# Performance work log

Hardware: AMD Instinct MI355X
Metric: run time of the kernel (lower is better)

## Reference

```python
import jax, jax.numpy as jnp
import numpy as np

B = 512          # batch
T_STEPS = 32     # clip_length (loop runs T-1 = 32 times)
BELIEF = 1024
STATE = 256
HIDDEN = 1024
EMB = 1024
POSE_TILES = 1
MIN_STD = 0.1


def setup_inputs() -> dict:
    key = jax.random.key(0)
    ks = jax.random.split(key, 24)
    s = 0.02
    rn = lambda k, sh: (jax.random.normal(k, sh, dtype=jnp.float32) * s)
    d = {
        "prev_state": jax.random.normal(ks[0], (B, STATE), dtype=jnp.float32),
        "prev_belief": jax.random.normal(ks[1], (B, BELIEF), dtype=jnp.float32),
        "poses": jax.random.normal(ks[2], (T_STEPS, B, 6), dtype=jnp.float32),
        "observations": jax.random.normal(ks[3], (T_STEPS, B, EMB), dtype=jnp.float32),
        "post_noise": jax.random.normal(ks[4], (T_STEPS, B, STATE), dtype=jnp.float32),
        "prior_noise": jax.random.normal(ks[5], (T_STEPS, B, STATE), dtype=jnp.float32),
        # fc_embed_state: 2*state -> belief
        "w_es": rn(ks[6], (2 * STATE, BELIEF)), "b_es": jnp.zeros((BELIEF,), jnp.float32),
        # GRUCell(belief, belief); torch gate order r, z, n
        "w_ih": rn(ks[7], (BELIEF, 3 * BELIEF)), "w_hh": rn(ks[8], (BELIEF, 3 * BELIEF)),
        "b_ih": jnp.zeros((3 * BELIEF,), jnp.float32), "b_hh": jnp.zeros((3 * BELIEF,), jnp.float32),
        # fc_embed_belief_posterior: belief+emb -> hidden
        "w_ebpo": rn(ks[9], (BELIEF + EMB, HIDDEN)), "b_ebpo": jnp.zeros((HIDDEN,), jnp.float32),
        # fc_state_posterior: hidden -> 2*state
        "w_spo": rn(ks[10], (HIDDEN, 2 * STATE)), "b_spo": jnp.zeros((2 * STATE,), jnp.float32),
        # fc_embed_belief_prior: belief + 6*pose_tiles -> hidden
        "w_ebpr": rn(ks[11], (BELIEF + 6 * POSE_TILES, HIDDEN)), "b_ebpr": jnp.zeros((HIDDEN,), jnp.float32),
        # fc_state_prior: hidden -> 2*state
        "w_spr": rn(ks[12], (HIDDEN, 2 * STATE)), "b_spr": jnp.zeros((2 * STATE,), jnp.float32),
    }
    return d


def _rssm(prev_state, prev_belief, poses, observations, post_noise, prior_noise,
          w_es, b_es, w_ih, w_hh, b_ih, b_hh,
          w_ebpo, b_ebpo, w_spo, b_spo, w_ebpr, b_ebpr, w_spr, b_spr):
    def gru_cell(x, h):
        gi = x @ w_ih + b_ih
        gh = h @ w_hh + b_hh
        ir, iz, inn = jnp.split(gi, 3, axis=1)
        hr, hz, hn = jnp.split(gh, 3, axis=1)
        r = jax.nn.sigmoid(ir + hr)
        z = jax.nn.sigmoid(iz + hz)
        n = jnp.tanh(inn + r * hn)
        return (1.0 - z) * n + z * h

    def step(carry, xs):
        post_s, prior_s, belief = carry
        obs_t, pose_t, n_post, n_prior = xs
        hidden = jax.nn.relu(jnp.concatenate([post_s, prior_s], axis=1) @ w_es + b_es)
        belief = gru_cell(hidden, belief)
        # posterior branch
        hp = jax.nn.relu(jnp.concatenate([belief, obs_t], axis=1) @ w_ebpo + b_ebpo)
        pm, psd_raw = jnp.split(hp @ w_spo + b_spo, 2, axis=1)
        psd = jax.nn.softplus(psd_raw) + MIN_STD
        ps = pm + psd * n_post
        # prior branch (pose tiled)
        pose_rep = jnp.tile(pose_t, (1, POSE_TILES))
        hq = jax.nn.relu(jnp.concatenate([belief, pose_rep], axis=1) @ w_ebpr + b_ebpr)
        prm, prsd_raw = jnp.split(hq @ w_spr + b_spr, 2, axis=1)
        prsd = jax.nn.softplus(prsd_raw) + MIN_STD
        prs = prm + prsd * n_prior
        return (ps, prs, belief), (belief, prs, prm, prsd, ps, pm, psd)

    init = (prev_state, prev_state, prev_belief)
    _, outs = jax.lax.scan(step, init, (observations, poses, post_noise, prior_noise))
    # outs: beliefs, prior_states, prior_means, prior_std_devs, posterior_states, posterior_means, posterior_std_devs  (each [T-1, B, *])
    return outs


def reference(prev_state, prev_belief, poses, observations, post_noise, prior_noise,
              w_es, b_es, w_ih, w_hh, b_ih, b_hh,
              w_ebpo, b_ebpo, w_spo, b_spo, w_ebpr, b_ebpr, w_spr, b_spr):
    return _rssm(prev_state, prev_belief, poses, observations, post_noise, prior_noise,
                 w_es, b_es, w_ih, w_hh, b_ih, b_hh,
                 w_ebpo, b_ebpo, w_spo, b_spo, w_ebpr, b_ebpr, w_spr, b_spr)
```

## Files before the change

### kernel.cpp

```cpp
#include <hip/hip_runtime.h>
#include <math.h>


typedef __attribute__((ext_vector_type(8))) short bf16x8;
typedef __attribute__((ext_vector_type(4))) float f32x4;

#define MFMA(a, b, c) __builtin_amdgcn_mfma_f32_16x16x32_bf16(a, b, c, 0, 0, 0)
#define NBLK 256

__device__ __forceinline__ short f2bf(float f) {
    unsigned u = __float_as_uint(f);
    u += 0x7FFF + ((u >> 16) & 1);
    return (short)(u >> 16);
}
__device__ __forceinline__ float sigmoidf_(float x) { return 1.f / (1.f + expf(-x)); }
__device__ __forceinline__ float softplusf_(float x) {
    return fmaxf(x, 0.f) + log1pf(expf(-fabsf(x)));
}
__device__ __forceinline__ f32x4 zero4() { f32x4 v = {0.f, 0.f, 0.f, 0.f}; return v; }

__global__ __launch_bounds__(256) void k_swizzle(const float* __restrict__ W,
                                                 short* __restrict__ out,
                                                 int KT, int N)
{
    int gw = blockIdx.x * 4 + (threadIdx.x >> 6);
    int lane = threadIdx.x & 63;
    int nt = gw / KT, kt = gw % KT;
    const float* src = W + (size_t)(kt * 32 + (lane >> 4) * 8) * N + nt * 16 + (lane & 15);
    short tmp[8];
#pragma unroll
    for (int j = 0; j < 8; ++j) tmp[j] = f2bf(src[(size_t)j * N]);
    *(bf16x8*)(out + (((size_t)gw * 64 + lane) << 3)) = *(const bf16x8*)tmp;
}

__global__ __launch_bounds__(256) void k_obs2bf(const float* __restrict__ obs,
                                                short* __restrict__ out)
{
    size_t i = ((size_t)blockIdx.x * 256 + threadIdx.x) * 8;
    short tmp[8];
#pragma unroll
    for (int j = 0; j < 8; ++j) tmp[j] = f2bf(obs[i + j]);
    *(bf16x8*)(out + i) = *(const bf16x8*)tmp;
}

__global__ __launch_bounds__(256) void k_init(const float* __restrict__ prev_state,
                                              const float* __restrict__ prev_belief,
                                              short* __restrict__ stateCat0,
                                              short* __restrict__ belInit,
                                              unsigned* __restrict__ bar)
{
    int i = blockIdx.x * 256 + threadIdx.x;
    if (i < 4096) bar[i] = 0u;
    if (i < 262144) {
        int m = i >> 9, c = i & 511;
        stateCat0[i] = f2bf(prev_state[m * 256 + (c & 255)]);
    } else {
        int j = i - 262144;
        belInit[j] = f2bf(prev_belief[j]);
    }
}

__device__ __forceinline__ bf16x8 loadA16(const short* A, int m0, int kelem, int strideElems, int lane) {
    return *(const bf16x8*)(A + (size_t)(m0 + (lane & 15)) * strideElems + kelem + ((lane >> 4) << 3));
}
__device__ __forceinline__ bf16x8 loadB16(const short* Bsw, size_t tileIdx, int lane) {
    return *(const bf16x8*)(Bsw + ((tileIdx * 64 + lane) << 3));
}

__device__ __forceinline__ void xbar(unsigned* cnt, unsigned target)
{
    __syncthreads();
    if (threadIdx.x == 0) {
        __hip_atomic_fetch_add(cnt, 1u, __ATOMIC_RELAXED, __HIP_MEMORY_SCOPE_AGENT);
        while (__hip_atomic_load(cnt, __ATOMIC_RELAXED, __HIP_MEMORY_SCOPE_AGENT) < target)
            __builtin_amdgcn_s_sleep(4);
    }
    __syncthreads();
}

struct RP2 {
    const short *sw_es, *sw_ih, *sw_hh, *sw_ebpo, *sw_ebpr, *sw_spo, *sw_spr;
    const float *Wf_ebpr;
    const float *b_es, *b_ih, *b_hh, *b_ebpo, *b_ebpr, *b_spo, *b_spr;
    const float *prev_belief, *poses, *post_noise, *prior_noise;
    const short *obsBf;
    const short *belInit;
    short *hiddenB, *belB, *hpB, *hqB, *scB;
    float *beliefs, *priStates, *priMeans, *priStds, *postStates, *postMeans, *postStds;
    unsigned *bar;
};

__global__ __launch_bounds__(256, 1) void k_rssm2(RP2 p)
{
    int wid = threadIdx.x >> 6;
    int lane = threadIdx.x & 63;
    int q = lane >> 4, cl = lane & 15;

    __shared__ unsigned s_g, s_rank, s_P;
    if (threadIdx.x == 0) {
        unsigned x;
        asm volatile("s_getreg_b32 %0, hwreg(HW_REG_XCC_ID)" : "=s"(x));
        x &= 7u;
        s_g = x;
        s_rank = __hip_atomic_fetch_add(p.bar + 64 + x * 64, 1u,
                                        __ATOMIC_RELAXED, __HIP_MEMORY_SCOPE_AGENT);
    }
    __syncthreads();
    if (threadIdx.x == 0) {
        __hip_atomic_fetch_add(p.bar, 1u, __ATOMIC_RELAXED, __HIP_MEMORY_SCOPE_AGENT);
        while (__hip_atomic_load(p.bar, __ATOMIC_RELAXED, __HIP_MEMORY_SCOPE_AGENT) < NBLK)
            __builtin_amdgcn_s_sleep(4);
        s_P = __hip_atomic_load(p.bar + 64 + s_g * 64,
                                __ATOMIC_RELAXED, __HIP_MEMORY_SCOPE_AGENT);
    }
    __syncthreads();
    const unsigned g = s_g, P = s_P, rank = s_rank;
    const unsigned NSLOT = P * 4;
    const unsigned slot = rank * 4 + (unsigned)wid;
    const int R0 = (int)g * 64;
    unsigned* cnt = p.bar + 1024 + g * 64;
    unsigned bcount = 0;

#pragma unroll 1
    for (int t = 0; t < 32; ++t) {
        {
            const short* sc = p.scB + (size_t)t * 262144;
            short* hid = p.hiddenB + (size_t)t * 524288;
            for (unsigned u = slot; u < 128; u += NSLOT) {
                int mt = u >> 6, nt = u & 63;
                int m0 = R0 + mt * 32;
                f32x4 acc0 = zero4(), acc1 = zero4();
#pragma unroll 4
                for (int kt = 0; kt < 16; ++kt) {
                    bf16x8 a0 = loadA16(sc, m0,      kt * 32, 512, lane);
                    bf16x8 a1 = loadA16(sc, m0 + 16, kt * 32, 512, lane);
                    bf16x8 b  = loadB16(p.sw_es, (size_t)nt * 16 + kt, lane);
                    acc0 = MFMA(a0, b, acc0);
                    acc1 = MFMA(a1, b, acc1);
                }
                int n = nt * 16 + cl;
                float bn = p.b_es[n];
#pragma unroll
                for (int i = 0; i < 4; ++i) {
                    int m = m0 + q * 4 + i;
                    hid[(size_t)m * 1024 + n]        = f2bf(fmaxf(acc0[i] + bn, 0.f));
                    hid[(size_t)(m + 16) * 1024 + n] = f2bf(fmaxf(acc1[i] + bn, 0.f));
                }
            }
        }
        xbar(cnt, ++bcount * P);

        {
            const short* hid = p.hiddenB + (size_t)t * 524288;
            const short* belPrevBf = t ? p.belB + (size_t)(t - 1) * 524288 : p.belInit;
            const float* Pf32 = t ? (p.beliefs + (size_t)(t - 1) * 524288) : p.prev_belief;
            float* belT = p.beliefs + (size_t)t * 524288;
            short* belCurBf = p.belB + (size_t)t * 524288;
            for (unsigned u = slot; u < 128; u += NSLOT) {
                int mt = u >> 6, nt = u & 63;
                int m0 = R0 + mt * 32;
                f32x4 r0 = zero4(), r1 = zero4(), z0 = zero4(), z1 = zero4();
                f32x4 ni0 = zero4(), ni1 = zero4(), nh0 = zero4(), nh1 = zero4();
#pragma unroll 4
                for (int kt = 0; kt < 32; ++kt) {
                    bf16x8 a0 = loadA16(hid, m0,      kt * 32, 1024, lane);
                    bf16x8 a1 = loadA16(hid, m0 + 16, kt * 32, 1024, lane);
                    bf16x8 br = loadB16(p.sw_ih, (size_t)(0 * 64 + nt) * 32 + kt, lane);
                    bf16x8 bz = loadB16(p.sw_ih, (size_t)(1 * 64 + nt) * 32 + kt, lane);
                    bf16x8 bn = loadB16(p.sw_ih, (size_t)(2 * 64 + nt) * 32 + kt, lane);
                    r0 = MFMA(a0, br, r0);   r1 = MFMA(a1, br, r1);
                    z0 = MFMA(a0, bz, z0);   z1 = MFMA(a1, bz, z1);
                    ni0 = MFMA(a0, bn, ni0); ni1 = MFMA(a1, bn, ni1);
                }
#pragma unroll 4
                for (int kt = 0; kt < 32; ++kt) {
                    bf16x8 a0 = loadA16(belPrevBf, m0,      kt * 32, 1024, lane);
                    bf16x8 a1 = loadA16(belPrevBf, m0 + 16, kt * 32, 1024, lane);
                    bf16x8 br = loadB16(p.sw_hh, (size_t)(0 * 64 + nt) * 32 + kt, lane);
                    bf16x8 bz = loadB16(p.sw_hh, (size_t)(1 * 64 + nt) * 32 + kt, lane);
                    bf16x8 bn = loadB16(p.sw_hh, (size_t)(2 * 64 + nt) * 32 + kt, lane);
                    r0 = MFMA(a0, br, r0);   r1 = MFMA(a1, br, r1);
                    z0 = MFMA(a0, bz, z0);   z1 = MFMA(a1, bz, z1);
                    nh0 = MFMA(a0, bn, nh0); nh1 = MFMA(a1, bn, nh1);
                }
                int n = nt * 16 + cl;
                float bihr = p.b_ih[n] + p.b_hh[n];
                float bihz = p.b_ih[1024 + n] + p.b_hh[1024 + n];
                float bin = p.b_ih[2048 + n], bhn = p.b_hh[2048 + n];
#pragma unroll
                for (int f = 0; f < 2; ++f) {
#pragma unroll
                    for (int i = 0; i < 4; ++i) {
                        int m = m0 + f * 16 + q * 4 + i;
                        float rv = f ? r1[i] : r0[i];
                        float zv = f ? z1[i] : z0[i];
                        float niv = f ? ni1[i] : ni0[i];
                        float nhv = f ? nh1[i] : nh0[i];
                        float rr = sigmoidf_(rv + bihr);
                        float zz = sigmoidf_(zv + bihz);
                        float ng = tanhf(niv + bin + rr * (nhv + bhn));
                        float h = Pf32[(size_t)m * 1024 + n];
                        float v = (1.f - zz) * ng + zz * h;
                        belT[(size_t)m * 1024 + n] = v;
                        belCurBf[(size_t)m * 1024 + n] = f2bf(v);
                    }
                }
            }
        }
        xbar(cnt, ++bcount * P);

        {
            const short* belCur = p.belB + (size_t)t * 524288;
            const short* obsT = p.obsBf + (size_t)t * 524288;
            const float* poseT = p.poses + (size_t)t * 3072;
            short* hp = p.hpB + (size_t)t * 524288;
            short* hq = p.hqB + (size_t)t * 524288;
            for (unsigned u = slot; u < 256; u += NSLOT) {
                int u2 = u & 127;
                int mt = u2 >> 6, nt = u2 & 63;
                int m0 = R0 + mt * 32;
                if (u < 128) {
                    f32x4 acc0 = zero4(), acc1 = zero4();
#pragma unroll 4
                    for (int kt = 0; kt < 32; ++kt) {
                        bf16x8 a0 = loadA16(belCur, m0,      kt * 32, 1024, lane);
                        bf16x8 a1 = loadA16(belCur, m0 + 16, kt * 32, 1024, lane);
                        bf16x8 bb = loadB16(p.sw_ebpo, (size_t)nt * 64 + kt, lane);
                        acc0 = MFMA(a0, bb, acc0);
                        acc1 = MFMA(a1, bb, acc1);
                    }
#pragma unroll 4
                    for (int kt = 32; kt < 64; ++kt) {
                        bf16x8 a0 = loadA16(obsT, m0,      (kt - 32) * 32, 1024, lane);
                        bf16x8 a1 = loadA16(obsT, m0 + 16, (kt - 32) * 32, 1024, lane);
                        bf16x8 bb = loadB16(p.sw_ebpo, (size_t)nt * 64 + kt, lane);
                        acc0 = MFMA(a0, bb, acc0);
                        acc1 = MFMA(a1, bb, acc1);
                    }
                    int n = nt * 16 + cl;
                    float bn = p.b_ebpo[n];
#pragma unroll
                    for (int i = 0; i < 4; ++i) {
                        int m = m0 + q * 4 + i;
                        hp[(size_t)m * 1024 + n]        = f2bf(fmaxf(acc0[i] + bn, 0.f));
                        hp[(size_t)(m + 16) * 1024 + n] = f2bf(fmaxf(acc1[i] + bn, 0.f));
                    }
                } else {
                    f32x4 acc0 = zero4(), acc1 = zero4();
#pragma unroll 4
                    for (int kt = 0; kt < 32; ++kt) {
                        bf16x8 a0 = loadA16(belCur, m0,      kt * 32, 1024, lane);
                        bf16x8 a1 = loadA16(belCur, m0 + 16, kt * 32, 1024, lane);
                        bf16x8 bb = loadB16(p.sw_ebpr, (size_t)nt * 32 + kt, lane);
                        acc0 = MFMA(a0, bb, acc0);
                        acc1 = MFMA(a1, bb, acc1);
                    }
                    int n = nt * 16 + cl;
                    float bn2 = p.b_ebpr[n];
#pragma unroll
                    for (int f = 0; f < 2; ++f) {
#pragma unroll
                        for (int i = 0; i < 4; ++i) {
                            int m = m0 + f * 16 + q * 4 + i;
                            float v = (f ? acc1[i] : acc0[i]) + bn2;
#pragma unroll
                            for (int pp = 0; pp < 6; ++pp)
                                v += poseT[(size_t)m * 6 + pp] * p.Wf_ebpr[(size_t)(1024 + pp) * 1024 + n];
                            hq[(size_t)m * 1024 + n] = f2bf(fmaxf(v, 0.f));
                        }
                    }
                }
            }
        }
        xbar(cnt, ++bcount * P);

        {
            const short* hp = p.hpB + (size_t)t * 524288;
            const short* hq = p.hqB + (size_t)t * 524288;
            short* scW = p.scB + (size_t)(t + 1) * 262144;
            for (unsigned u = slot; u < 128; u += NSLOT) {
                int br = u >> 6;
                int rem = u & 63;
                int mtd = rem >> 4;
                int ct = rem & 15;
                int mh = R0 + mtd * 16;
                const short* A = br ? hq : hp;
                const short* Bsw = br ? p.sw_spr : p.sw_spo;
                const float* bias = br ? p.b_spr : p.b_spo;
                const float* noise = (br ? p.prior_noise : p.post_noise) + (size_t)t * 131072;
                float* mO  = (br ? p.priMeans  : p.postMeans)  + (size_t)t * 131072;
                float* sO  = (br ? p.priStds   : p.postStds)   + (size_t)t * 131072;
                float* stO = (br ? p.priStates : p.postStates) + (size_t)t * 131072;
                int catOff = br ? 256 : 0;
                f32x4 ma = zero4(), sa = zero4();
#pragma unroll 4
                for (int kt = 0; kt < 32; ++kt) {
                    bf16x8 a  = loadA16(A, mh, kt * 32, 1024, lane);
                    bf16x8 bm = loadB16(Bsw, (size_t)ct * 32 + kt, lane);
                    bf16x8 bs = loadB16(Bsw, (size_t)(16 + ct) * 32 + kt, lane);
                    ma = MFMA(a, bm, ma);
                    sa = MFMA(a, bs, sa);
                }
#pragma unroll
                for (int i = 0; i < 4; ++i) {
                    int m = mh + q * 4 + i;
                    int c = ct * 16 + cl;
                    float mean = ma[i] + bias[c];
                    float sd = softplusf_(sa[i] + bias[c + 256]) + 0.1f;
                    float st = mean + sd * noise[(size_t)m * 256 + c];
                    mO[(size_t)m * 256 + c] = mean;
                    sO[(size_t)m * 256 + c] = sd;
                    stO[(size_t)m * 256 + c] = st;
                    scW[(size_t)m * 512 + catOff + c] = f2bf(st);
                }
            }
        }
        xbar(cnt, ++bcount * P);
    }
}

__global__ __launch_bounds__(256) void k_embed_state(
    const short* __restrict__ A, const short* __restrict__ Bsw,
    const float* __restrict__ bias, short* __restrict__ outBf)
{
    int wid = threadIdx.x >> 6;
    int lane = threadIdx.x & 63;
    int nt = blockIdx.x & 63, mb = blockIdx.x >> 6;
    int m0 = (mb * 4 + wid) * 32;
    f32x4 acc0 = zero4(), acc1 = zero4();
#pragma unroll 4
    for (int kt = 0; kt < 16; ++kt) {
        bf16x8 a0 = loadA16(A, m0,      kt * 32, 512, lane);
        bf16x8 a1 = loadA16(A, m0 + 16, kt * 32, 512, lane);
        bf16x8 b  = loadB16(Bsw, (size_t)nt * 16 + kt, lane);
        acc0 = MFMA(a0, b, acc0);
        acc1 = MFMA(a1, b, acc1);
    }
    int q = lane >> 4, cl = lane & 15;
    int n = nt * 16 + cl;
    float bn = bias[n];
#pragma unroll
    for (int i = 0; i < 4; ++i) {
        int m = m0 + q * 4 + i;
        outBf[(size_t)m * 1024 + n]        = f2bf(fmaxf(acc0[i] + bn, 0.f));
        outBf[(size_t)(m + 16) * 1024 + n] = f2bf(fmaxf(acc1[i] + bn, 0.f));
    }
}

__global__ __launch_bounds__(256) void k_gru(
    const short* __restrict__ Hbf, const short* __restrict__ Pbf,
    const float* __restrict__ Pf32,
    const short* __restrict__ sw_ih, const short* __restrict__ sw_hh,
    const float* __restrict__ b_ih, const float* __restrict__ b_hh,
    float* __restrict__ belF32, short* __restrict__ belBf)
{
    int wid = threadIdx.x >> 6;
    int lane = threadIdx.x & 63;
    int nt = blockIdx.x & 63, mb = blockIdx.x >> 6;
    int m0 = (mb * 4 + wid) * 32;
    f32x4 r0 = zero4(), r1 = zero4(), z0 = zero4(), z1 = zero4();
    f32x4 ni0 = zero4(), ni1 = zero4(), nh0 = zero4(), nh1 = zero4();
#pragma unroll 4
    for (int kt = 0; kt < 32; ++kt) {
        bf16x8 a0 = loadA16(Hbf, m0,      kt * 32, 1024, lane);
        bf16x8 a1 = loadA16(Hbf, m0 + 16, kt * 32, 1024, lane);
        bf16x8 br = loadB16(sw_ih, (size_t)(0 * 64 + nt) * 32 + kt, lane);
        bf16x8 bz = loadB16(sw_ih, (size_t)(1 * 64 + nt) * 32 + kt, lane);
        bf16x8 bn = loadB16(sw_ih, (size_t)(2 * 64 + nt) * 32 + kt, lane);
        r0 = MFMA(a0, br, r0);   r1 = MFMA(a1, br, r1);
        z0 = MFMA(a0, bz, z0);   z1 = MFMA(a1, bz, z1);
        ni0 = MFMA(a0, bn, ni0); ni1 = MFMA(a1, bn, ni1);
    }
#pragma unroll 4
    for (int kt = 0; kt < 32; ++kt) {
        bf16x8 a0 = loadA16(Pbf, m0,      kt * 32, 1024, lane);
        bf16x8 a1 = loadA16(Pbf, m0 + 16, kt * 32, 1024, lane);
        bf16x8 br = loadB16(sw_hh, (size_t)(0 * 64 + nt) * 32 + kt, lane);
        bf16x8 bz = loadB16(sw_hh, (size_t)(1 * 64 + nt) * 32 + kt, lane);
        bf16x8 bn = loadB16(sw_hh, (size_t)(2 * 64 + nt) * 32 + kt, lane);
        r0 = MFMA(a0, br, r0);   r1 = MFMA(a1, br, r1);
        z0 = MFMA(a0, bz, z0);   z1 = MFMA(a1, bz, z1);
        nh0 = MFMA(a0, bn, nh0); nh1 = MFMA(a1, bn, nh1);
    }
    int q = lane >> 4, cl = lane & 15;
    int n = nt * 16 + cl;
    float bihr = b_ih[n] + b_hh[n];
    float bihz = b_ih[1024 + n] + b_hh[1024 + n];
    float bin = b_ih[2048 + n], bhn = b_hh[2048 + n];
#pragma unroll
    for (int f = 0; f < 2; ++f) {
#pragma unroll
        for (int i = 0; i < 4; ++i) {
            int m = m0 + f * 16 + q * 4 + i;
            float rv = f ? r1[i] : r0[i];
            float zv = f ? z1[i] : z0[i];
            float niv = f ? ni1[i] : ni0[i];
            float nhv = f ? nh1[i] : nh0[i];
            float rr = sigmoidf_(rv + bihr);
            float zz = sigmoidf_(zv + bihz);
            float ng = tanhf(niv + bin + rr * (nhv + bhn));
            float h = Pf32[(size_t)m * 1024 + n];
            float v = (1.f - zz) * ng + zz * h;
            belF32[(size_t)m * 1024 + n] = v;
            belBf[(size_t)m * 1024 + n] = f2bf(v);
        }
    }
}

__global__ __launch_bounds__(256) void k_pp(
    const short* __restrict__ Bel, const short* __restrict__ ObsBf,
    const float* __restrict__ Pose,
    const short* __restrict__ sw_ebpo, const short* __restrict__ sw_ebpr,
    const float* __restrict__ Wf_ebpr,
    const float* __restrict__ b_ebpo, const float* __restrict__ b_ebpr,
    short* __restrict__ hpBf, short* __restrict__ hqBf)
{
    int wid = threadIdx.x >> 6;
    int lane = threadIdx.x & 63;
    int q = lane >> 4, cl = lane & 15;
    int b = blockIdx.x;
    if (b < 256) {
        int nt = b & 63, mb = b >> 6;
        int m0 = (mb * 4 + wid) * 32;
        f32x4 acc0 = zero4(), acc1 = zero4();
#pragma unroll 4
        for (int kt = 0; kt < 32; ++kt) {
            bf16x8 a0 = loadA16(Bel, m0,      kt * 32, 1024, lane);
            bf16x8 a1 = loadA16(Bel, m0 + 16, kt * 32, 1024, lane);
            bf16x8 bb = loadB16(sw_ebpo, (size_t)nt * 64 + kt, lane);
            acc0 = MFMA(a0, bb, acc0);
            acc1 = MFMA(a1, bb, acc1);
        }
#pragma unroll 4
        for (int kt = 32; kt < 64; ++kt) {
            bf16x8 a0 = loadA16(ObsBf, m0,      (kt - 32) * 32, 1024, lane);
            bf16x8 a1 = loadA16(ObsBf, m0 + 16, (kt - 32) * 32, 1024, lane);
            bf16x8 bb = loadB16(sw_ebpo, (size_t)nt * 64 + kt, lane);
            acc0 = MFMA(a0, bb, acc0);
            acc1 = MFMA(a1, bb, acc1);
        }
        int n = nt * 16 + cl;
        float bn = b_ebpo[n];
#pragma unroll
        for (int i = 0; i < 4; ++i) {
            int m = m0 + q * 4 + i;
            hpBf[(size_t)m * 1024 + n]        = f2bf(fmaxf(acc0[i] + bn, 0.f));
            hpBf[(size_t)(m + 16) * 1024 + n] = f2bf(fmaxf(acc1[i] + bn, 0.f));
        }
    } else {
        int b2 = b - 256;
        int nt = b2 & 63, mb = b2 >> 6;
        int m0 = (mb * 4 + wid) * 32;
        f32x4 acc0 = zero4(), acc1 = zero4();
#pragma unroll 4
        for (int kt = 0; kt < 32; ++kt) {
            bf16x8 a0 = loadA16(Bel, m0,      kt * 32, 1024, lane);
            bf16x8 a1 = loadA16(Bel, m0 + 16, kt * 32, 1024, lane);
            bf16x8 bb = loadB16(sw_ebpr, (size_t)nt * 32 + kt, lane);
            acc0 = MFMA(a0, bb, acc0);
            acc1 = MFMA(a1, bb, acc1);
        }
        int n = nt * 16 + cl;
        float bn = b_ebpr[n];
#pragma unroll
        for (int f = 0; f < 2; ++f) {
#pragma unroll
            for (int i = 0; i < 4; ++i) {
                int m = m0 + f * 16 + q * 4 + i;
                float v = (f ? acc1[i] : acc0[i]) + bn;
#pragma unroll
                for (int pp = 0; pp < 6; ++pp)
                    v += Pose[(size_t)m * 6 + pp] * Wf_ebpr[(size_t)(1024 + pp) * 1024 + n];
                hqBf[(size_t)m * 1024 + n] = f2bf(fmaxf(v, 0.f));
            }
        }
    }
}

__global__ __launch_bounds__(256) void k_head(
    const short* __restrict__ Hp, const short* __restrict__ Hq,
    const short* __restrict__ sw_spo, const short* __restrict__ sw_spr,
    const float* __restrict__ b_spo, const float* __restrict__ b_spr,
    const float* __restrict__ nPost, const float* __restrict__ nPri,
    float* __restrict__ pM, float* __restrict__ pS, float* __restrict__ pSt,
    float* __restrict__ qM, float* __restrict__ qS, float* __restrict__ qSt,
    short* __restrict__ stateCat)
{
    int gw = blockIdx.x * 4 + (threadIdx.x >> 6);
    int lane = threadIdx.x & 63;
    int br = gw >> 9, rem = gw & 511;
    int mt = rem >> 4, ct = rem & 15;
    int m0 = mt * 16;
    const short* A = br ? Hq : Hp;
    const short* Bsw = br ? sw_spr : sw_spo;
    const float* bias = br ? b_spr : b_spo;
    const float* noise = br ? nPri : nPost;
    float* mO = br ? qM : pM;
    float* sO = br ? qS : pS;
    float* stO = br ? qSt : pSt;
    int catOff = br ? 256 : 0;
    f32x4 ma = zero4(), sa = zero4();
#pragma unroll 4
    for (int kt = 0; kt < 32; ++kt) {
        bf16x8 a = loadA16(A, m0, kt * 32, 1024, lane);
        bf16x8 bm = loadB16(Bsw, (size_t)ct * 32 + kt, lane);
        bf16x8 bs = loadB16(Bsw, (size_t)(16 + ct) * 32 + kt, lane);
        ma = MFMA(a, bm, ma);
        sa = MFMA(a, bs, sa);
    }
    int q = lane >> 4, cl = lane & 15;
#pragma unroll
    for (int i = 0; i < 4; ++i) {
        int m = m0 + q * 4 + i;
        int c = ct * 16 + cl;
        float mean = ma[i] + bias[c];
        float sd = softplusf_(sa[i] + bias[c + 256]) + 0.1f;
        float st = mean + sd * noise[(size_t)m * 256 + c];
        mO[(size_t)m * 256 + c] = mean;
        sO[(size_t)m * 256 + c] = sd;
        stO[(size_t)m * 256 + c] = st;
        stateCat[(size_t)m * 512 + catOff + c] = f2bf(st);
    }
}

extern "C" void kernel_launch(void* const* d_in, const int* in_sizes, int n_in,
                              void* d_out, int out_size, void* d_ws, size_t ws_size,
                              hipStream_t stream)
{
    const float* prev_state  = (const float*)d_in[0];
    const float* prev_belief = (const float*)d_in[1];
    const float* poses       = (const float*)d_in[2];
    const float* obs         = (const float*)d_in[3];
    const float* post_noise  = (const float*)d_in[4];
    const float* prior_noise = (const float*)d_in[5];
    const float* w_es   = (const float*)d_in[6];
    const float* b_es   = (const float*)d_in[7];
    const float* w_ih   = (const float*)d_in[8];
    const float* w_hh   = (const float*)d_in[9];
    const float* b_ih   = (const float*)d_in[10];
    const float* b_hh   = (const float*)d_in[11];
    const float* w_ebpo = (const float*)d_in[12];
    const float* b_ebpo = (const float*)d_in[13];
    const float* w_spo  = (const float*)d_in[14];
    const float* b_spo  = (const float*)d_in[15];
    const float* w_ebpr = (const float*)d_in[16];
    const float* b_ebpr = (const float*)d_in[17];
    const float* w_spr  = (const float*)d_in[18];
    const float* b_spr  = (const float*)d_in[19];

    float* out = (float*)d_out;
    float* beliefs    = out;
    float* priStates  = out + 16777216;
    float* priMeans   = out + 20971520;
    float* priStds    = out + 25165824;
    float* postStates = out + 29360128;
    float* postMeans  = out + 33554432;
    float* postStds   = out + 37748736;

    short* ws = (short*)d_ws;
    size_t o = 0;
    short* sw_es   = ws + o; o += (size_t)512 * 1024;
    short* sw_ih   = ws + o; o += (size_t)1024 * 3072;
    short* sw_hh   = ws + o; o += (size_t)1024 * 3072;
    short* sw_ebpo = ws + o; o += (size_t)2048 * 1024;
    short* sw_ebpr = ws + o; o += (size_t)1024 * 1024;
    short* sw_spo  = ws + o; o += (size_t)1024 * 512;
    short* sw_spr  = ws + o; o += (size_t)1024 * 512;
    short* obsBf   = ws + o; o += (size_t)32 * 512 * 1024;
    short* hiddenB = ws + o; o += (size_t)32 * 512 * 1024;
    short* belInit = ws + o; o += (size_t)512 * 1024;
    short* belB    = ws + o; o += (size_t)32 * 512 * 1024;
    short* hpB     = ws + o; o += (size_t)32 * 512 * 1024;
    short* hqB     = ws + o; o += (size_t)32 * 512 * 1024;
    short* scB     = ws + o; o += (size_t)33 * 512 * 512;
    unsigned* bar  = (unsigned*)(ws + o); o += 8192;

    k_swizzle<<<dim3(256),  dim3(256), 0, stream>>>(w_es,   sw_es,   16, 1024);
    k_swizzle<<<dim3(1536), dim3(256), 0, stream>>>(w_ih,   sw_ih,   32, 3072);
    k_swizzle<<<dim3(1536), dim3(256), 0, stream>>>(w_hh,   sw_hh,   32, 3072);
    k_swizzle<<<dim3(1024), dim3(256), 0, stream>>>(w_ebpo, sw_ebpo, 64, 1024);
    k_swizzle<<<dim3(512),  dim3(256), 0, stream>>>(w_ebpr, sw_ebpr, 32, 1024);
    k_swizzle<<<dim3(256),  dim3(256), 0, stream>>>(w_spo,  sw_spo,  32, 512);
    k_swizzle<<<dim3(256),  dim3(256), 0, stream>>>(w_spr,  sw_spr,  32, 512);
    k_obs2bf<<<dim3(8192), dim3(256), 0, stream>>>(obs, obsBf);
    k_init<<<dim3(3072), dim3(256), 0, stream>>>(prev_state, prev_belief, scB, belInit, bar);

    RP2 rp;
    rp.sw_es = sw_es; rp.sw_ih = sw_ih; rp.sw_hh = sw_hh;
    rp.sw_ebpo = sw_ebpo; rp.sw_ebpr = sw_ebpr; rp.sw_spo = sw_spo; rp.sw_spr = sw_spr;
    rp.Wf_ebpr = w_ebpr;
    rp.b_es = b_es; rp.b_ih = b_ih; rp.b_hh = b_hh;
    rp.b_ebpo = b_ebpo; rp.b_ebpr = b_ebpr; rp.b_spo = b_spo; rp.b_spr = b_spr;
    rp.prev_belief = prev_belief; rp.poses = poses;
    rp.post_noise = post_noise; rp.prior_noise = prior_noise;
    rp.obsBf = obsBf; rp.belInit = belInit;
    rp.hiddenB = hiddenB; rp.belB = belB; rp.hpB = hpB; rp.hqB = hqB; rp.scB = scB;
    rp.beliefs = beliefs;
    rp.priStates = priStates; rp.priMeans = priMeans; rp.priStds = priStds;
    rp.postStates = postStates; rp.postMeans = postMeans; rp.postStds = postStds;
    rp.bar = bar;

    void* kargs[] = { (void*)&rp };
    hipError_t ce = hipLaunchCooperativeKernel(k_rssm2, dim3(NBLK), dim3(256),
                                               kargs, 0u, stream);
    if (ce != hipSuccess) {
        for (int t = 0; t < 32; ++t) {
            const short* belPrevBf = t ? belB + (size_t)(t - 1) * 524288 : belInit;
            short* belCurBf = belB + (size_t)t * 524288;
            const float* belPrevF = t ? (beliefs + (size_t)(t - 1) * 524288) : prev_belief;
            float* belT = beliefs + (size_t)t * 524288;
            short* hid = hiddenB + (size_t)t * 524288;
            short* hp = hpB + (size_t)t * 524288;
            short* hq = hqB + (size_t)t * 524288;

            k_embed_state<<<dim3(256), dim3(256), 0, stream>>>(scB + (size_t)t * 262144,
                                                               sw_es, b_es, hid);
            k_gru<<<dim3(256), dim3(256), 0, stream>>>(hid, belPrevBf, belPrevF,
                                                       sw_ih, sw_hh, b_ih, b_hh, belT, belCurBf);
            k_pp<<<dim3(512), dim3(256), 0, stream>>>(belCurBf, obsBf + (size_t)t * 524288,
                                                      poses + (size_t)t * 3072,
                                                      sw_ebpo, sw_ebpr, w_ebpr,
                                                      b_ebpo, b_ebpr, hp, hq);
            k_head<<<dim3(256), dim3(256), 0, stream>>>(hp, hq, sw_spo, sw_spr, b_spo, b_spr,
                                                        post_noise + (size_t)t * 131072,
                                                        prior_noise + (size_t)t * 131072,
                                                        postMeans + (size_t)t * 131072,
                                                        postStds + (size_t)t * 131072,
                                                        postStates + (size_t)t * 131072,
                                                        priMeans + (size_t)t * 131072,
                                                        priStds + (size_t)t * 131072,
                                                        priStates + (size_t)t * 131072,
                                                        scB + (size_t)(t + 1) * 262144);
        }
    }
}
```

Baseline: 3.024 ms.

## Partition by output columns per XCD with hierarchical grid barrier and 512-thread blocks

The work split changes from per-XCD row partitions, each using all weight columns, to per-XCD column partitions covering all rows. Each XCD then streams only its own slice of the weights, which keeps those weights resident in its L2 cache. Because every step now needs data produced by other XCDs, the per-XCD barrier becomes a two-level grid barrier (local arrive, leader cross-XCD sync, local release), and intermediate stores use agent-scope atomic stores so other XCDs can see them. Block size doubles to 512 threads with 16-row MFMA tiles. In exchange, the A operand is no longer reused across two 16-row tiles, and each barrier now costs a global round trip.

```diff
diff --git a/kernel.cpp b/kernel.cpp
--- a/kernel.cpp
+++ b/kernel.cpp
@@ -18,6 +18,13 @@
     return fmaxf(x, 0.f) + log1pf(expf(-fabsf(x)));
 }
 __device__ __forceinline__ f32x4 zero4() { f32x4 v = {0.f, 0.f, 0.f, 0.f}; return v; }
+
+__device__ __forceinline__ void stS(short* p, short v) {
+    __hip_atomic_store(p, v, __ATOMIC_RELAXED, __HIP_MEMORY_SCOPE_AGENT);
+}
+__device__ __forceinline__ unsigned ldU(const unsigned* p) {
+    return __hip_atomic_load(p, __ATOMIC_RELAXED, __HIP_MEMORY_SCOPE_AGENT);
+}
 
 __global__ __launch_bounds__(256) void k_swizzle(const float* __restrict__ W,
                                                  short* __restrict__ out,
@@ -65,17 +72,6 @@
 }
 __device__ __forceinline__ bf16x8 loadB16(const short* Bsw, size_t tileIdx, int lane) {
     return *(const bf16x8*)(Bsw + ((tileIdx * 64 + lane) << 3));
-}
-
-__device__ __forceinline__ void xbar(unsigned* cnt, unsigned target)
-{
-    __syncthreads();
-    if (threadIdx.x == 0) {
-        __hip_atomic_fetch_add(cnt, 1u, __ATOMIC_RELAXED, __HIP_MEMORY_SCOPE_AGENT);
-        while (__hip_atomic_load(cnt, __ATOMIC_RELAXED, __HIP_MEMORY_SCOPE_AGENT) < target)
-            __builtin_amdgcn_s_sleep(4);
-    }
-    __syncthreads();
 }
 
 struct RP2 {
@@ -90,7 +86,28 @@
     unsigned *bar;
 };
 
-__global__ __launch_bounds__(256, 1) void k_rssm2(RP2 p)
+__device__ __forceinline__ void hbar(unsigned* bar, unsigned g, unsigned P,
+                                     unsigned rank, unsigned* bc)
+{
+    unsigned c = ++(*bc);
+    __syncthreads();
+    if (threadIdx.x == 0) {
+        unsigned* larr = bar + 1024 + g * 64;
+        unsigned* lrel = bar + 2048 + g * 64;
+        __hip_atomic_fetch_add(larr, 1u, __ATOMIC_RELAXED, __HIP_MEMORY_SCOPE_AGENT);
+        if (rank == 0) {
+            while (ldU(larr) < c * P) {}
+            __hip_atomic_fetch_add(bar + 8, 1u, __ATOMIC_RELAXED, __HIP_MEMORY_SCOPE_AGENT);
+            while (ldU(bar + 8) < c * 8u) {}
+            __hip_atomic_store(lrel, c, __ATOMIC_RELAXED, __HIP_MEMORY_SCOPE_AGENT);
+        } else {
+            while (ldU(lrel) < c) {}
+        }
+    }
+    __syncthreads();
+}
+
+__global__ __launch_bounds__(512, 1) void k_rssm3(RP2 p)
 {
     int wid = threadIdx.x >> 6;
     int lane = threadIdx.x & 63;
@@ -108,47 +125,40 @@
     __syncthreads();
     if (threadIdx.x == 0) {
         __hip_atomic_fetch_add(p.bar, 1u, __ATOMIC_RELAXED, __HIP_MEMORY_SCOPE_AGENT);
-        while (__hip_atomic_load(p.bar, __ATOMIC_RELAXED, __HIP_MEMORY_SCOPE_AGENT) < NBLK)
-            __builtin_amdgcn_s_sleep(4);
-        s_P = __hip_atomic_load(p.bar + 64 + s_g * 64,
-                                __ATOMIC_RELAXED, __HIP_MEMORY_SCOPE_AGENT);
+        while (ldU(p.bar) < NBLK) {}
+        s_P = ldU(p.bar + 64 + s_g * 64);
     }
     __syncthreads();
     const unsigned g = s_g, P = s_P, rank = s_rank;
-    const unsigned NSLOT = P * 4;
-    const unsigned slot = rank * 4 + (unsigned)wid;
-    const int R0 = (int)g * 64;
-    unsigned* cnt = p.bar + 1024 + g * 64;
-    unsigned bcount = 0;
+    const unsigned NSLOT = P * 8;
+    const unsigned slot = rank * 8 + (unsigned)wid;
+    unsigned bc = 0;
 
 #pragma unroll 1
     for (int t = 0; t < 32; ++t) {
         {
             const short* sc = p.scB + (size_t)t * 262144;
             short* hid = p.hiddenB + (size_t)t * 524288;
-            for (unsigned u = slot; u < 128; u += NSLOT) {
-                int mt = u >> 6, nt = u & 63;
-                int m0 = R0 + mt * 32;
-                f32x4 acc0 = zero4(), acc1 = zero4();
+            for (unsigned u = slot; u < 256; u += NSLOT) {
+                int mt = (int)(u >> 3), ntl = (int)(u & 7);
+                int nt = (int)g * 8 + ntl;
+                int m0 = mt * 16;
+                f32x4 acc = zero4();
 #pragma unroll 4
                 for (int kt = 0; kt < 16; ++kt) {
-                    bf16x8 a0 = loadA16(sc, m0,      kt * 32, 512, lane);
-                    bf16x8 a1 = loadA16(sc, m0 + 16, kt * 32, 512, lane);
-                    bf16x8 b  = loadB16(p.sw_es, (size_t)nt * 16 + kt, lane);
-                    acc0 = MFMA(a0, b, acc0);
-                    acc1 = MFMA(a1, b, acc1);
+                    bf16x8 a = loadA16(sc, m0, kt * 32, 512, lane);
+                    bf16x8 b = loadB16(p.sw_es, (size_t)nt * 16 + kt, lane);
+                    acc = MFMA(a, b, acc);
                 }
                 int n = nt * 16 + cl;
                 float bn = p.b_es[n];
 #pragma unroll
-                for (int i = 0; i < 4; ++i) {
-                    int m = m0 + q * 4 + i;
-                    hid[(size_t)m * 1024 + n]        = f2bf(fmaxf(acc0[i] + bn, 0.f));
-                    hid[(size_t)(m + 16) * 1024 + n] = f2bf(fmaxf(acc1[i] + bn, 0.f));
-                }
+                for (int i = 0; i < 4; ++i)
+                    stS(&hid[(size_t)(m0 + q * 4 + i) * 1024 + n],
+                        f2bf(fmaxf(acc[i] + bn, 0.f)));
             }
         }
-        xbar(cnt, ++bcount * P);
+        hbar(p.bar, g, P, rank, &bc);
 
         {
             const short* hid = p.hiddenB + (size_t)t * 524288;
@@ -156,58 +166,49 @@
             const float* Pf32 = t ? (p.beliefs + (size_t)(t - 1) * 524288) : p.prev_belief;
             float* belT = p.beliefs + (size_t)t * 524288;
             short* belCurBf = p.belB + (size_t)t * 524288;
-            for (unsigned u = slot; u < 128; u += NSLOT) {
-                int mt = u >> 6, nt = u & 63;
-                int m0 = R0 + mt * 32;
-                f32x4 r0 = zero4(), r1 = zero4(), z0 = zero4(), z1 = zero4();
-                f32x4 ni0 = zero4(), ni1 = zero4(), nh0 = zero4(), nh1 = zero4();
+            for (unsigned u = slot; u < 256; u += NSLOT) {
+                int mt = (int)(u >> 3), ntl = (int)(u & 7);
+                int nt = (int)g * 8 + ntl;
+                int m0 = mt * 16;
+                f32x4 r = zero4(), z = zero4(), ni = zero4(), nh = zero4();
 #pragma unroll 4
                 for (int kt = 0; kt < 32; ++kt) {
-                    bf16x8 a0 = loadA16(hid, m0,      kt * 32, 1024, lane);
-                    bf16x8 a1 = loadA16(hid, m0 + 16, kt * 32, 1024, lane);
+                    bf16x8 a  = loadA16(hid, m0, kt * 32, 1024, lane);
                     bf16x8 br = loadB16(p.sw_ih, (size_t)(0 * 64 + nt) * 32 + kt, lane);
                     bf16x8 bz = loadB16(p.sw_ih, (size_t)(1 * 64 + nt) * 32 + kt, lane);
                     bf16x8 bn = loadB16(p.sw_ih, (size_t)(2 * 64 + nt) * 32 + kt, lane);
-                    r0 = MFMA(a0, br, r0);   r1 = MFMA(a1, br, r1);
-                    z0 = MFMA(a0, bz, z0);   z1 = MFMA(a1, bz, z1);
-                    ni0 = MFMA(a0, bn, ni0); ni1 = MFMA(a1, bn, ni1);
+                    r = MFMA(a, br, r);
+                    z = MFMA(a, bz, z);
+                    ni = MFMA(a, bn, ni);
                 }
 #pragma unroll 4
                 for (int kt = 0; kt < 32; ++kt) {
-                    bf16x8 a0 = loadA16(belPrevBf, m0,      kt * 32, 1024, lane);
-                    bf16x8 a1 = loadA16(belPrevBf, m0 + 16, kt * 32, 1024, lane);
+                    bf16x8 a  = loadA16(belPrevBf, m0, kt * 32, 1024, lane);
                     bf16x8 br = loadB16(p.sw_hh, (size_t)(0 * 64 + nt) * 32 + kt, lane);
                     bf16x8 bz = loadB16(p.sw_hh, (size_t)(1 * 64 + nt) * 32 + kt, lane);
                     bf16x8 bn = loadB16(p.sw_hh, (size_t)(2 * 64 + nt) * 32 + kt, lane);
-                    r0 = MFMA(a0, br, r0);   r1 = MFMA(a1, br, r1);
-                    z0 = MFMA(a0, bz, z0);   z1 = MFMA(a1, bz, z1);
-                    nh0 = MFMA(a0, bn, nh0); nh1 = MFMA(a1, bn, nh1);
+                    r = MFMA(a, br, r);
+                    z = MFMA(a, bz, z);
+                    nh = MFMA(a, bn, nh);
                 }
                 int n = nt * 16 + cl;
                 float bihr = p.b_ih[n] + p.b_hh[n];
                 float bihz = p.b_ih[1024 + n] + p.b_hh[1024 + n];
                 float bin = p.b_ih[2048 + n], bhn = p.b_hh[2048 + n];
 #pragma unroll
-                for (int f = 0; f < 2; ++f) {
-#pragma unroll
-                    for (int i = 0; i < 4; ++i) {
-                        int m = m0 + f * 16 + q * 4 + i;
-                        float rv = f ? r1[i] : r0[i];
-                        float zv = f ? z1[i] : z0[i];
-                        float niv = f ? ni1[i] : ni0[i];
-                        float nhv = f ? nh1[i] : nh0[i];
-                        float rr = sigmoidf_(rv + bihr);
-                        float zz = sigmoidf_(zv + bihz);
-                        float ng = tanhf(niv + bin + rr * (nhv + bhn));
-                        float h = Pf32[(size_t)m * 1024 + n];
-                        float v = (1.f - zz) * ng + zz * h;
-                        belT[(size_t)m * 1024 + n] = v;
-                        belCurBf[(size_t)m * 1024 + n] = f2bf(v);
-                    }
+                for (int i = 0; i < 4; ++i) {
+                    int m = m0 + q * 4 + i;
+                    float rr = sigmoidf_(r[i] + bihr);
+                    float zz = sigmoidf_(z[i] + bihz);
+                    float ng = tanhf(ni[i] + bin + rr * (nh[i] + bhn));
+                    float h = Pf32[(size_t)m * 1024 + n];
+                    float v = (1.f - zz) * ng + zz * h;
+                    belT[(size_t)m * 1024 + n] = v;
+                    stS(&belCurBf[(size_t)m * 1024 + n], f2bf(v));
                 }
             }
         }
-        xbar(cnt, ++bcount * P);
+        hbar(p.bar, g, P, rank, &bc);
 
         {
             const short* belCur = p.belB + (size_t)t * 524288;
@@ -215,75 +216,65 @@
             const float* poseT = p.poses + (size_t)t * 3072;
             short* hp = p.hpB + (size_t)t * 524288;
             short* hq = p.hqB + (size_t)t * 524288;
-            for (unsigned u = slot; u < 256; u += NSLOT) {
-                int u2 = u & 127;
-                int mt = u2 >> 6, nt = u2 & 63;
-                int m0 = R0 + mt * 32;
-                if (u < 128) {
-                    f32x4 acc0 = zero4(), acc1 = zero4();
+            for (unsigned u = slot; u < 512; u += NSLOT) {
+                unsigned u2 = u & 255;
+                int mt = (int)(u2 >> 3), ntl = (int)(u2 & 7);
+                int nt = (int)g * 8 + ntl;
+                int m0 = mt * 16;
+                int n = nt * 16 + cl;
+                if (u < 256) {
+                    f32x4 acc = zero4();
 #pragma unroll 4
                     for (int kt = 0; kt < 32; ++kt) {
-                        bf16x8 a0 = loadA16(belCur, m0,      kt * 32, 1024, lane);
-                        bf16x8 a1 = loadA16(belCur, m0 + 16, kt * 32, 1024, lane);
-                        bf16x8 bb = loadB16(p.sw_ebpo, (size_t)nt * 64 + kt, lane);
-                        acc0 = MFMA(a0, bb, acc0);
-                        acc1 = MFMA(a1, bb, acc1);
+                        bf16x8 a = loadA16(belCur, m0, kt * 32, 1024, lane);
+                        bf16x8 b = loadB16(p.sw_ebpo, (size_t)nt * 64 + kt, lane);
+                        acc = MFMA(a, b, acc);
                     }
 #pragma unroll 4
                     for (int kt = 32; kt < 64; ++kt) {
-                        bf16x8 a0 = loadA16(obsT, m0,      (kt - 32) * 32, 1024, lane);
-                        bf16x8 a1 = loadA16(obsT, m0 + 16, (kt - 32) * 32, 1024, lane);
-                        bf16x8 bb = loadB16(p.sw_ebpo, (size_t)nt * 64 + kt, lane);
-                        acc0 = MFMA(a0, bb, acc0);
-                        acc1 = MFMA(a1, bb, acc1);
+                        bf16x8 a = loadA16(obsT, m0, (kt - 32) * 32, 1024, lane);
+                        bf16x8 b = loadB16(p.sw_ebpo, (size_t)nt * 64 + kt, lane);
+                        acc = MFMA(a, b, acc);
                     }
-                    int n = nt * 16 + cl;
                     float bn = p.b_ebpo[n];
+#pragma unroll
+                    for (int i = 0; i < 4; ++i)
+                        stS(&hp[(size_t)(m0 + q * 4 + i) * 1024 + n],
+                            f2bf(fmaxf(acc[i] + bn, 0.f)));
+                } else {
+                    f32x4 acc = zero4();
+#pragma unroll 4
+                    for (int kt = 0; kt < 32; ++kt) {
+                        bf16x8 a = loadA16(belCur, m0, kt * 32, 1024, lane);
+                        bf16x8 b = loadB16(p.sw_ebpr, (size_t)nt * 32 + kt, lane);
+                        acc = MFMA(a, b, acc);
+                    }
+                    float bn2 = p.b_ebpr[n];
 #pragma unroll
                     for (int i = 0; i < 4; ++i) {
                         int m = m0 + q * 4 + i;
-                        hp[(size_t)m * 1024 + n]        = f2bf(fmaxf(acc0[i] + bn, 0.f));
-                        hp[(size_t)(m + 16) * 1024 + n] = f2bf(fmaxf(acc1[i] + bn, 0.f));
-                    }
-                } else {
-                    f32x4 acc0 = zero4(), acc1 = zero4();
-#pragma unroll 4
-                    for (int kt = 0; kt < 32; ++kt) {
-                        bf16x8 a0 = loadA16(belCur, m0,      kt * 32, 1024, lane);
-                        bf16x8 a1 = loadA16(belCur, m0 + 16, kt * 32, 1024, lane);
-                        bf16x8 bb = loadB16(p.sw_ebpr, (size_t)nt * 32 + kt, lane);
-                        acc0 = MFMA(a0, bb, acc0);
-                        acc1 = MFMA(a1, bb, acc1);
-                    }
-                    int n = nt * 16 + cl;
-                    float bn2 = p.b_ebpr[n];
-#pragma unroll
-                    for (int f = 0; f < 2; ++f) {
-#pragma unroll
-                        for (int i = 0; i < 4; ++i) {
-                            int m = m0 + f * 16 + q * 4 + i;
-                            float v = (f ? acc1[i] : acc0[i]) + bn2;
-#pragma unroll
-                            for (int pp = 0; pp < 6; ++pp)
-                                v += poseT[(size_t)m * 6 + pp] * p.Wf_ebpr[(size_t)(1024 + pp) * 1024 + n];
-                            hq[(size_t)m * 1024 + n] = f2bf(fmaxf(v, 0.f));
-                        }
+                        float v = acc[i] + bn2;
+#pragma unroll
+                        for (int pp = 0; pp < 6; ++pp)
+                            v += poseT[(size_t)m * 6 + pp] * p.Wf_ebpr[(size_t)(1024 + pp) * 1024 + n];
+                        stS(&hq[(size_t)m * 1024 + n], f2bf(fmaxf(v, 0.f)));
                     }
                 }
             }
         }
-        xbar(cnt, ++bcount * P);
+        hbar(p.bar, g, P, rank, &bc);
 
         {
             const short* hp = p.hpB + (size_t)t * 524288;
             const short* hq = p.hqB + (size_t)t * 524288;
             short* scW = p.scB + (size_t)(t + 1) * 262144;
             for (unsigned u = slot; u < 128; u += NSLOT) {
-                int br = u >> 6;
-                int rem = u & 63;
-                int mtd = rem >> 4;
-                int ct = rem & 15;
-                int mh = R0 + mtd * 16;
+                int br = (int)(u >> 6);
+                int rem = (int)(u & 63);
+                int mt = rem >> 1;
+                int ctl = rem & 1;
+                int ct = (int)g * 2 + ctl;
+                int mh = mt * 16;
                 const short* A = br ? hq : hp;
                 const short* Bsw = br ? p.sw_spr : p.sw_spo;
                 const float* bias = br ? p.b_spr : p.b_spo;
@@ -311,11 +302,11 @@
                     mO[(size_t)m * 256 + c] = mean;
                     sO[(size_t)m * 256 + c] = sd;
                     stO[(size_t)m * 256 + c] = st;
-                    scW[(size_t)m * 512 + catOff + c] = f2bf(st);
+                    stS(&scW[(size_t)m * 512 + catOff + c], f2bf(st));
                 }
             }
         }
-        xbar(cnt, ++bcount * P);
+        hbar(p.bar, g, P, rank, &bc);
     }
 }
 
@@ -601,7 +592,7 @@
     rp.bar = bar;
 
     void* kargs[] = { (void*)&rp };
-    hipError_t ce = hipLaunchCooperativeKernel(k_rssm2, dim3(NBLK), dim3(256),
+    hipError_t ce = hipLaunchCooperativeKernel(k_rssm3, dim3(NBLK), dim3(512),
                                                kargs, 0u, stream);
     if (ce != hipSuccess) {
         for (int t = 0; t < 32; ++t) {
```

New measurement: 3.377 ms, median of 2. +11.7%, slower.
